# Performance work log

Measured on AMD Instinct MI355X. Metric: run time of the kernel, lower is better.

Reference implementation:

```python
import jax, jax.numpy as jnp
import numpy as np

N, L, K, D = 131072, 8, 1024, 1024


def setup_inputs() -> dict:
    key = jax.random.key(0)
    k1, k2 = jax.random.split(key)
    x = jax.random.randint(k1, (N, L), 0, K, dtype=jnp.int32)
    weight = jax.random.normal(k2, (L, K, D), dtype=jnp.float32)
    return {"x": x, "weight": weight}


def reference(x, weight):
    # Original: one-hot(x) -> [N, L, K]; einsum('l k d, n l k -> n d', w, oh)
    # == sum over levels of a direct embedding gather:
    #   out[n] = sum_l weight[l, x[n, l], :]
    L_ = weight.shape[0]
    gathered = weight[jnp.arange(L_)[None, :], x, :]  # [N, L, D]
    return gathered.sum(axis=1)  # [N, D]
```

## Files before the change

### kernel.cpp

```cpp
#include <hip/hip_runtime.h>


#define N_ROWS 131072
#define L_DIM 8
#define K_DIM 1024
#define D_DIM 1024

#define NXCD 8
#define ROWS_PER_BLOCK 128
#define CHUNKS (N_ROWS / ROWS_PER_BLOCK)
#define W_ELEMS (L_DIM * K_DIM * D_DIM)

typedef float        f32x4 __attribute__((ext_vector_type(4)));
typedef unsigned int u32x2 __attribute__((ext_vector_type(2)));

__device__ __forceinline__ unsigned short f2bf_rne(float f) {
    unsigned u = __float_as_uint(f);
    unsigned r = u + 0x7fffu + ((u >> 16) & 1u);
    return (unsigned short)(r >> 16);
}
__device__ __forceinline__ float bflo(unsigned u) { return __uint_as_float(u << 16); }
__device__ __forceinline__ float bfhi(unsigned u) { return __uint_as_float(u & 0xffff0000u); }

__global__ __launch_bounds__(256) void convert_w_bf16(
    const float* __restrict__ w, unsigned short* __restrict__ wb)
{
    const int i = blockIdx.x * 256 + threadIdx.x;
    const f32x4 v = __builtin_nontemporal_load(
        reinterpret_cast<const f32x4*>(w) + i);
    ushort4 o;
    o.x = f2bf_rne(v.x); o.y = f2bf_rne(v.y);
    o.z = f2bf_rne(v.z); o.w = f2bf_rne(v.w);
    reinterpret_cast<ushort4*>(wb)[i] = o;
}

__global__ __launch_bounds__(256) void gather_sum_bf16(
    const int* __restrict__ x,
    const unsigned short* __restrict__ wb,
    float* __restrict__ out)
{
    __shared__ int sxi[ROWS_PER_BLOCK * L_DIM];

    const int slice = blockIdx.x & (NXCD - 1);
    const int chunk = blockIdx.x >> 3;
    const int t     = threadIdx.x;
    const int n0    = chunk * ROWS_PER_BLOCK;

    reinterpret_cast<int4*>(sxi)[t] =
        reinterpret_cast<const int4*>(x + (size_t)n0 * L_DIM)[t];
    __syncthreads();

    const int rg   = t >> 5;
    const int lane = t & 31;
    const int col  = slice * 128 + lane * 4;
    const unsigned colb = (unsigned)col * 2u;
    const char* __restrict__ wbytes = (const char*)wb;

    #pragma unroll
    for (int i = 0; i < 4; ++i) {
        u32x2 v[4][L_DIM];
        #pragma unroll
        for (int j = 0; j < 4; ++j) {
            const int r = rg + 8 * (4 * i + j);
            const int* __restrict__ xr = sxi + r * L_DIM;
            #pragma unroll
            for (int l = 0; l < L_DIM; ++l) {
                const unsigned off = colb +
                    (((unsigned)(l * K_DIM) + (unsigned)xr[l]) << 11);
                v[j][l] = *reinterpret_cast<const u32x2*>(wbytes + off);
            }
        }

        #pragma unroll
        for (int j = 0; j < 4; ++j) {
            const int r = rg + 8 * (4 * i + j);
            f32x4 acc = (f32x4)(0.f);
            #pragma unroll
            for (int l = 0; l < L_DIM; ++l) {
                acc.x += bflo(v[j][l][0]); acc.y += bfhi(v[j][l][0]);
                acc.z += bflo(v[j][l][1]); acc.w += bfhi(v[j][l][1]);
            }
            __builtin_nontemporal_store(acc,
                reinterpret_cast<f32x4*>(out + (size_t)(n0 + r) * D_DIM + col));
        }
    }
}

__global__ __launch_bounds__(256) void gather_sum_f32(
    const int* __restrict__ x,
    const float* __restrict__ w,
    float* __restrict__ out)
{
    __shared__ int sxi[ROWS_PER_BLOCK * L_DIM];
    const int slice = blockIdx.x & (NXCD - 1);
    const int chunk = blockIdx.x >> 3;
    const int t     = threadIdx.x;
    const int n0    = chunk * ROWS_PER_BLOCK;

    reinterpret_cast<int4*>(sxi)[t] =
        reinterpret_cast<const int4*>(x + (size_t)n0 * L_DIM)[t];
    __syncthreads();

    const int rg   = t >> 5;
    const int lane = t & 31;
    const int col  = slice * 128 + lane * 4;
    const float* __restrict__ wbase = w + col;

    #pragma unroll
    for (int i = 0; i < 8; ++i) {
        const int rA = rg + 16 * i;
        const int rB = rA + 8;
        const int* xA = sxi + rA * L_DIM;
        const int* xB = sxi + rB * L_DIM;
        f32x4 vA[L_DIM], vB[L_DIM];
        #pragma unroll
        for (int l = 0; l < L_DIM; ++l)
            vA[l] = *reinterpret_cast<const f32x4*>(
                wbase + (size_t)(l * K_DIM + xA[l]) * D_DIM);
        #pragma unroll
        for (int l = 0; l < L_DIM; ++l)
            vB[l] = *reinterpret_cast<const f32x4*>(
                wbase + (size_t)(l * K_DIM + xB[l]) * D_DIM);
        f32x4 accA = ((vA[0] + vA[1]) + (vA[2] + vA[3]))
                   + ((vA[4] + vA[5]) + (vA[6] + vA[7]));
        f32x4 accB = ((vB[0] + vB[1]) + (vB[2] + vB[3]))
                   + ((vB[4] + vB[5]) + (vB[6] + vB[7]));
        __builtin_nontemporal_store(accA,
            reinterpret_cast<f32x4*>(out + (size_t)(n0 + rA) * D_DIM + col));
        __builtin_nontemporal_store(accB,
            reinterpret_cast<f32x4*>(out + (size_t)(n0 + rB) * D_DIM + col));
    }
}

extern "C" void kernel_launch(void* const* d_in, const int* in_sizes, int n_in,
                              void* d_out, int out_size, void* d_ws, size_t ws_size,
                              hipStream_t stream)
{
    const int*   x = (const int*)d_in[0];
    const float* w = (const float*)d_in[1];
    float* out = (float*)d_out;

    if (ws_size >= (size_t)W_ELEMS * 2) {
        unsigned short* wb = (unsigned short*)d_ws;
        convert_w_bf16<<<W_ELEMS / 4 / 256, 256, 0, stream>>>(w, wb);
        gather_sum_bf16<<<CHUNKS * NXCD, 256, 0, stream>>>(x, wb, out);
    } else {
        gather_sum_f32<<<CHUNKS * NXCD, 256, 0, stream>>>(x, w, out);
    }
}
```

Measured before the change: 156.8 us.

## Stage bf16 weight gathers into LDS via async global_load_lds double buffering

```diff
diff --git a/kernel.cpp b/kernel.cpp
--- a/kernel.cpp
+++ b/kernel.cpp
@@ -7,8 +7,10 @@
 #define D_DIM 1024
 
 #define NXCD 8
-#define ROWS_PER_BLOCK 128
-#define CHUNKS (N_ROWS / ROWS_PER_BLOCK)
+#define RPB 128
+#define CR 16
+#define NCH (RPB / CR)
+#define GRID_CHUNKS (N_ROWS / RPB)
 #define W_ELEMS (L_DIM * K_DIM * D_DIM)
 
 typedef float        f32x4 __attribute__((ext_vector_type(4)));
@@ -22,6 +24,13 @@
 __device__ __forceinline__ float bflo(unsigned u) { return __uint_as_float(u << 16); }
 __device__ __forceinline__ float bfhi(unsigned u) { return __uint_as_float(u & 0xffff0000u); }
 
+__device__ __forceinline__ void load_lds16(const void* g, void* l) {
+    __builtin_amdgcn_global_load_lds(
+        (const __attribute__((address_space(1))) void*)g,
+        (__attribute__((address_space(3))) void*)l,
+        16, 0, 0);
+}
+
 __global__ __launch_bounds__(256) void convert_w_bf16(
     const float* __restrict__ w, unsigned short* __restrict__ wb)
 {
@@ -34,55 +43,85 @@
     reinterpret_cast<ushort4*>(wb)[i] = o;
 }
 
-__global__ __launch_bounds__(256) void gather_sum_bf16(
+__global__ __launch_bounds__(256) void gather_sum_dma(
     const int* __restrict__ x,
     const unsigned short* __restrict__ wb,
     float* __restrict__ out)
 {
-    __shared__ int sxi[ROWS_PER_BLOCK * L_DIM];
+    __shared__ int sxi[RPB * L_DIM];
+    __shared__ __align__(1024) char buf[2][CR * L_DIM * 256];
 
     const int slice = blockIdx.x & (NXCD - 1);
     const int chunk = blockIdx.x >> 3;
     const int t     = threadIdx.x;
-    const int n0    = chunk * ROWS_PER_BLOCK;
+    const int n0    = chunk * RPB;
 
-    reinterpret_cast<int4*>(sxi)[t] =
-        reinterpret_cast<const int4*>(x + (size_t)n0 * L_DIM)[t];
+    if (t < RPB * L_DIM / 4)
+        reinterpret_cast<int4*>(sxi)[t] =
+            reinterpret_cast<const int4*>(x + (size_t)n0 * L_DIM)[t];
     __syncthreads();
 
-    const int rg   = t >> 5;
+    const int w_id = t >> 6;
+    const int lam  = t & 63;
+    const int grp  = lam >> 4;
+    const int sub  = lam & 15;
+    const int half = (t >> 5) & 1;
     const int lane = t & 31;
-    const int col  = slice * 128 + lane * 4;
-    const unsigned colb = (unsigned)col * 2u;
+
+    const unsigned colb = (unsigned)slice << 8;
     const char* __restrict__ wbytes = (const char*)wb;
 
     #pragma unroll
-    for (int i = 0; i < 4; ++i) {
-        u32x2 v[4][L_DIM];
-        #pragma unroll
-        for (int j = 0; j < 4; ++j) {
-            const int r = rg + 8 * (4 * i + j);
-            const int* __restrict__ xr = sxi + r * L_DIM;
+    for (int i = 0; i < 8; ++i) {
+        const int j = w_id * 8 + i;
+        const int g = 4 * j + grp;
+        const int l = g & 7;
+        const int k = sxi[g];
+        const unsigned off = (((unsigned)((l << 10) + k)) << 11) + colb
+                           + (unsigned)sub * 16u;
+        load_lds16(wbytes + off, &buf[0][j * 1024]);
+    }
+    __syncthreads();
+
+    #pragma unroll
+    for (int c = 0; c < NCH; ++c) {
+        if (c + 1 < NCH) {
             #pragma unroll
-            for (int l = 0; l < L_DIM; ++l) {
-                const unsigned off = colb +
-                    (((unsigned)(l * K_DIM) + (unsigned)xr[l]) << 11);
-                v[j][l] = *reinterpret_cast<const u32x2*>(wbytes + off);
+            for (int i = 0; i < 8; ++i) {
+                const int j = w_id * 8 + i;
+                const int g = 4 * j + grp;
+                const int l = g & 7;
+                const int k = sxi[(c + 1) * 128 + g];
+                const unsigned off = (((unsigned)((l << 10) + k)) << 11) + colb
+                                   + (unsigned)sub * 16u;
+                load_lds16(wbytes + off, &buf[(c + 1) & 1][j * 1024]);
             }
         }
 
+        const char* __restrict__ rb = buf[c & 1];
         #pragma unroll
-        for (int j = 0; j < 4; ++j) {
-            const int r = rg + 8 * (4 * i + j);
+        for (int s = 0; s < 2; ++s) {
+            const int r = w_id * 4 + s * 2 + half;
+            u32x2 v[L_DIM];
+            #pragma unroll
+            for (int l = 0; l < L_DIM; ++l)
+                v[l] = *reinterpret_cast<const u32x2*>(
+                    rb + (r * 8 + l) * 256 + lane * 8);
+
             f32x4 acc = (f32x4)(0.f);
             #pragma unroll
             for (int l = 0; l < L_DIM; ++l) {
-                acc.x += bflo(v[j][l][0]); acc.y += bfhi(v[j][l][0]);
-                acc.z += bflo(v[j][l][1]); acc.w += bfhi(v[j][l][1]);
+                acc.x += bflo(v[l][0]); acc.y += bfhi(v[l][0]);
+                acc.z += bflo(v[l][1]); acc.w += bfhi(v[l][1]);
             }
+
+            const int n = n0 + c * CR + r;
             __builtin_nontemporal_store(acc,
-                reinterpret_cast<f32x4*>(out + (size_t)(n0 + r) * D_DIM + col));
+                reinterpret_cast<f32x4*>(
+                    out + (size_t)n * D_DIM + slice * 128 + lane * 4));
         }
+
+        __syncthreads();
     }
 }
 
@@ -91,14 +130,15 @@
     const float* __restrict__ w,
     float* __restrict__ out)
 {
-    __shared__ int sxi[ROWS_PER_BLOCK * L_DIM];
+    __shared__ int sxi[RPB * L_DIM];
     const int slice = blockIdx.x & (NXCD - 1);
     const int chunk = blockIdx.x >> 3;
     const int t     = threadIdx.x;
-    const int n0    = chunk * ROWS_PER_BLOCK;
+    const int n0    = chunk * RPB;
 
-    reinterpret_cast<int4*>(sxi)[t] =
-        reinterpret_cast<const int4*>(x + (size_t)n0 * L_DIM)[t];
+    if (t < RPB * L_DIM / 4)
+        reinterpret_cast<int4*>(sxi)[t] =
+            reinterpret_cast<const int4*>(x + (size_t)n0 * L_DIM)[t];
     __syncthreads();
 
     const int rg   = t >> 5;
@@ -143,8 +183,8 @@
     if (ws_size >= (size_t)W_ELEMS * 2) {
         unsigned short* wb = (unsigned short*)d_ws;
         convert_w_bf16<<<W_ELEMS / 4 / 256, 256, 0, stream>>>(w, wb);
-        gather_sum_bf16<<<CHUNKS * NXCD, 256, 0, stream>>>(x, wb, out);
+        gather_sum_dma<<<GRID_CHUNKS * NXCD, 256, 0, stream>>>(x, wb, out);
     } else {
-        gather_sum_f32<<<CHUNKS * NXCD, 256, 0, stream>>>(x, w, out);
+        gather_sum_f32<<<GRID_CHUNKS * NXCD, 256, 0, stream>>>(x, w, out);
     }
 }
```

After: 152.6 us. 1.03x faster.
